# Kernel tuning notes

Hardware: AMD Instinct MI355X
Metric: run time of the kernel (lower is better)

## Reference

```python
import jax, jax.numpy as jnp
import numpy as np

EMBED_DIM = 1024
NUM_HEADS = 16
HEAD_DIM = EMBED_DIM // NUM_HEADS
MLP_SIZE = 4096
LN_EPS = 1e-5


def setup_inputs() -> dict:
    key = jax.random.key(0)
    ks = jax.random.split(key, 12)
    d, f = EMBED_DIM, MLP_SIZE
    s = lambda fan_in: 1.0 / np.sqrt(fan_in)
    return {
        "x": jax.random.normal(ks[0], (2, 2048, d), dtype=jnp.float32),
        "ln1_g": jnp.ones((d,), jnp.float32),
        "ln1_b": jnp.zeros((d,), jnp.float32),
        "ln2_g": jnp.ones((d,), jnp.float32),
        "ln2_b": jnp.zeros((d,), jnp.float32),
        "w_qkv": jax.random.uniform(ks[1], (d, 3 * d), jnp.float32, -s(d), s(d)),
        "b_qkv": jax.random.uniform(ks[2], (3 * d,), jnp.float32, -s(d), s(d)),
        "w_proj": jax.random.uniform(ks[3], (d, d), jnp.float32, -s(d), s(d)),
        "b_proj": jax.random.uniform(ks[4], (d,), jnp.float32, -s(d), s(d)),
        "w_fc1": jax.random.uniform(ks[5], (d, f), jnp.float32, -s(d), s(d)),
        "b_fc1": jax.random.uniform(ks[6], (f,), jnp.float32, -s(d), s(d)),
        "w_fc2": jax.random.uniform(ks[7], (f, d), jnp.float32, -s(f), s(f)),
        "b_fc2": jax.random.uniform(ks[8], (d,), jnp.float32, -s(f), s(f)),
    }


def _layernorm(x, g, b):
    mu = jnp.mean(x, axis=-1, keepdims=True)
    var = jnp.mean(jnp.square(x - mu), axis=-1, keepdims=True)
    return (x - mu) * jax.lax.rsqrt(var + LN_EPS) * g + b


def reference(x, ln1_g, ln1_b, ln2_g, ln2_b, w_qkv, b_qkv, w_proj, b_proj,
              w_fc1, b_fc1, w_fc2, b_fc2):
    B, N, C = x.shape
    H, D = NUM_HEADS, HEAD_DIM
    scale = D ** -0.5

    # --- attention sub-block (pre-LN) ---
    h = _layernorm(x, ln1_g, ln1_b)
    qkv = h @ w_qkv + b_qkv                      # [B,N,3C]
    qkv = qkv.reshape(B, N, 3, H, D)
    q, k, v = (jnp.moveaxis(qkv, 2, 0)[i].transpose(0, 2, 1, 3) for i in range(3))  # each [B,H,N,D]
    attn = jnp.einsum("bhnd,bhmd->bhnm", q, k) * scale
    attn = jax.nn.softmax(attn, axis=-1)
    o = jnp.einsum("bhnm,bhmd->bhnd", attn, v)   # [B,H,N,D]
    o = o.transpose(0, 2, 1, 3).reshape(B, N, C)
    x = x + (o @ w_proj + b_proj)

    # --- MLP sub-block (pre-LN) ---
    h = _layernorm(x, ln2_g, ln2_b)
    h = jax.nn.gelu(h @ w_fc1 + b_fc1, approximate=False)
    x = x + (h @ w_fc2 + b_fc2)
    return x
```

## Files before the change

kernel.cpp:

```cpp
#include <hip/hip_runtime.h>
#include <hip/hip_bf16.h>

typedef __attribute__((ext_vector_type(8))) __bf16 bf16x8;
typedef __attribute__((ext_vector_type(4))) float f32x4;
typedef unsigned short u16;

__device__ __forceinline__ float bf2f(u16 u) {
    unsigned int i = ((unsigned int)u) << 16;
    return __builtin_bit_cast(float, i);
}
__device__ __forceinline__ u16 f2bf_u16(float f) {
    __hip_bfloat16 h = __float2bfloat16(f);
    return *(u16*)&h;
}
__device__ __forceinline__ float gelu_f(float v) {
    return 0.5f * v * (1.0f + erff(v * 0.70710678118654752440f));
}
__device__ __forceinline__ bf16x8 ld_bf8_b64x2(const u16* p) {
    uint2 lo = *(const uint2*)p;
    uint2 hi = *(const uint2*)(p + 4);
    uint4 v = make_uint4(lo.x, lo.y, hi.x, hi.y);
    return __builtin_bit_cast(bf16x8, v);
}
__device__ __forceinline__ void async16(const void* g, void* l) {
    __builtin_amdgcn_global_load_lds(
        (const __attribute__((address_space(1))) void*)g,
        (__attribute__((address_space(3))) void*)l, 16, 0, 0);
}

__global__ void detect_dtype(const void* __restrict__ g1, int* __restrict__ flag) {
    unsigned v = *(const unsigned*)g1;
    *flag = (v == 0x3F800000u) ? 1 : 0;
}

__device__ __forceinline__ void conv8(const void* src, u16* dst, long off, bool f32in) {
    if (f32in) {
        const float* s = (const float*)src + off;
        float4 a = *(const float4*)s, b = *(const float4*)(s + 4);
        u16 o[8] = {f2bf_u16(a.x), f2bf_u16(a.y), f2bf_u16(a.z), f2bf_u16(a.w),
                    f2bf_u16(b.x), f2bf_u16(b.y), f2bf_u16(b.z), f2bf_u16(b.w)};
        *(uint4*)(dst + off) = *(const uint4*)o;
    } else {
        *(uint4*)(dst + off) = *(const uint4*)((const u16*)src + off);
    }
}

__global__ __launch_bounds__(256) void conv_bias(
        const void* __restrict__ bq, const void* __restrict__ bp,
        const void* __restrict__ b1, const void* __restrict__ b2,
        u16* dbq, u16* dbp, u16* db1, u16* db2,
        const int* __restrict__ flag) {
    long e = ((long)blockIdx.x * 256 + threadIdx.x) * 8;
    if (e >= 9216L) return;
    bool f = (*flag != 0);
    if      (e < 3072L) conv8(bq, dbq, e, f);
    else if (e < 4096L) conv8(bp, dbp, e - 3072L, f);
    else if (e < 8192L) conv8(b1, db1, e - 4096L, f);
    else                conv8(b2, db2, e - 8192L, f);
}

__global__ __launch_bounds__(256) void conv_t(const void* __restrict__ src,
                                              u16* __restrict__ dst,
                                              int K, int N,
                                              const int* __restrict__ flag) {
    const bool f32in = (*flag != 0);
    __shared__ u16 T[64 * 68];
    int k0 = blockIdx.y * 64, n0 = blockIdx.x * 64;
    int t = threadIdx.x;
    int kr = t >> 2, nc = (t & 3) * 16;

    u16 tmp[16];
    if (f32in) {
        const float* s = (const float*)src + (size_t)(k0 + kr) * N + n0 + nc;
        float4 a = *(const float4*)s;
        float4 b = *(const float4*)(s + 4);
        float4 c = *(const float4*)(s + 8);
        float4 d = *(const float4*)(s + 12);
        tmp[0]=f2bf_u16(a.x);  tmp[1]=f2bf_u16(a.y);  tmp[2]=f2bf_u16(a.z);  tmp[3]=f2bf_u16(a.w);
        tmp[4]=f2bf_u16(b.x);  tmp[5]=f2bf_u16(b.y);  tmp[6]=f2bf_u16(b.z);  tmp[7]=f2bf_u16(b.w);
        tmp[8]=f2bf_u16(c.x);  tmp[9]=f2bf_u16(c.y);  tmp[10]=f2bf_u16(c.z); tmp[11]=f2bf_u16(c.w);
        tmp[12]=f2bf_u16(d.x); tmp[13]=f2bf_u16(d.y); tmp[14]=f2bf_u16(d.z); tmp[15]=f2bf_u16(d.w);
    } else {
        const u16* s = (const u16*)src + (size_t)(k0 + kr) * N + n0 + nc;
        *(uint4*)&tmp[0] = *(const uint4*)s;
        *(uint4*)&tmp[8] = *(const uint4*)(s + 8);
    }
    u16* dl = &T[kr * 68 + nc];
    #pragma unroll
    for (int j = 0; j < 4; ++j)
        *(uint2*)(dl + 4 * j) = *(const uint2*)&tmp[4 * j];
    __syncthreads();

    int nr = t >> 2, kc = (t & 3) * 16;
    u16 o[16];
    #pragma unroll
    for (int i = 0; i < 16; ++i) o[i] = T[(kc + i) * 68 + nr];
    u16* dp = dst + (size_t)(n0 + nr) * K + k0 + kc;
    *(uint4*)dp       = *(const uint4*)&o[0];
    *(uint4*)(dp + 8) = *(const uint4*)&o[8];
}

__global__ __launch_bounds__(256) void ln_first(const void* __restrict__ xin,
                                                const void* __restrict__ g,
                                                const void* __restrict__ b,
                                                __hip_bfloat16* __restrict__ out,
                                                const int* __restrict__ flag) {
    const bool f32in = (*flag != 0);
    int row = blockIdx.x, t = threadIdx.x;
    size_t base = (size_t)row * 1024 + 4 * t;
    float v[4];
    if (f32in) {
        float4 f = *(const float4*)((const float*)xin + base);
        v[0] = f.x; v[1] = f.y; v[2] = f.z; v[3] = f.w;
    } else {
        ushort4 u = *(const ushort4*)((const __hip_bfloat16*)xin + base);
        v[0] = bf2f(u.x); v[1] = bf2f(u.y); v[2] = bf2f(u.z); v[3] = bf2f(u.w);
    }
    float s = v[0] + v[1] + v[2] + v[3];
    float s2 = v[0]*v[0] + v[1]*v[1] + v[2]*v[2] + v[3]*v[3];
    #pragma unroll
    for (int off = 32; off > 0; off >>= 1) {
        s  += __shfl_down(s, off);
        s2 += __shfl_down(s2, off);
    }
    __shared__ float red[8];
    int wave = t >> 6, lane = t & 63;
    if (lane == 0) { red[wave] = s; red[4 + wave] = s2; }
    __syncthreads();
    float S  = red[0] + red[1] + red[2] + red[3];
    float S2 = red[4] + red[5] + red[6] + red[7];
    float mean = S * (1.0f / 1024.0f);
    float var  = S2 * (1.0f / 1024.0f) - mean * mean;
    float rstd = rsqrtf(var + 1e-5f);
    float gg[4], bb[4];
    if (f32in) {
        float4 fg = *(const float4*)((const float*)g + 4 * t);
        float4 fb = *(const float4*)((const float*)b + 4 * t);
        gg[0]=fg.x; gg[1]=fg.y; gg[2]=fg.z; gg[3]=fg.w;
        bb[0]=fb.x; bb[1]=fb.y; bb[2]=fb.z; bb[3]=fb.w;
    } else {
        ushort4 ug = *(const ushort4*)((const __hip_bfloat16*)g + 4 * t);
        ushort4 ub = *(const ushort4*)((const __hip_bfloat16*)b + 4 * t);
        gg[0]=bf2f(ug.x); gg[1]=bf2f(ug.y); gg[2]=bf2f(ug.z); gg[3]=bf2f(ug.w);
        bb[0]=bf2f(ub.x); bb[1]=bf2f(ub.y); bb[2]=bf2f(ub.z); bb[3]=bf2f(ub.w);
    }
    #pragma unroll
    for (int i = 0; i < 4; ++i)
        out[base + i] = __float2bfloat16((v[i] - mean) * rstd * gg[i] + bb[i]);
}

__global__ __launch_bounds__(256) void ln_mid(const float* __restrict__ x,
                                              const void* __restrict__ g,
                                              const void* __restrict__ b,
                                              __hip_bfloat16* __restrict__ out,
                                              const int* __restrict__ flag) {
    const bool f32in = (*flag != 0);
    int row = blockIdx.x, t = threadIdx.x;
    size_t base = (size_t)row * 1024 + 4 * t;
    float4 f = *(const float4*)(x + base);
    float v[4] = {f.x, f.y, f.z, f.w};
    float s = v[0] + v[1] + v[2] + v[3];
    float s2 = v[0]*v[0] + v[1]*v[1] + v[2]*v[2] + v[3]*v[3];
    #pragma unroll
    for (int off = 32; off > 0; off >>= 1) {
        s  += __shfl_down(s, off);
        s2 += __shfl_down(s2, off);
    }
    __shared__ float red[8];
    int wave = t >> 6, lane = t & 63;
    if (lane == 0) { red[wave] = s; red[4 + wave] = s2; }
    __syncthreads();
    float S  = red[0] + red[1] + red[2] + red[3];
    float S2 = red[4] + red[5] + red[6] + red[7];
    float mean = S * (1.0f / 1024.0f);
    float var  = S2 * (1.0f / 1024.0f) - mean * mean;
    float rstd = rsqrtf(var + 1e-5f);
    float gg[4], bb[4];
    if (f32in) {
        float4 fg = *(const float4*)((const float*)g + 4 * t);
        float4 fb = *(const float4*)((const float*)b + 4 * t);
        gg[0]=fg.x; gg[1]=fg.y; gg[2]=fg.z; gg[3]=fg.w;
        bb[0]=fb.x; bb[1]=fb.y; bb[2]=fb.z; bb[3]=fb.w;
    } else {
        ushort4 ug = *(const ushort4*)((const __hip_bfloat16*)g + 4 * t);
        ushort4 ub = *(const ushort4*)((const __hip_bfloat16*)b + 4 * t);
        gg[0]=bf2f(ug.x); gg[1]=bf2f(ug.y); gg[2]=bf2f(ug.z); gg[3]=bf2f(ug.w);
        bb[0]=bf2f(ub.x); bb[1]=bf2f(ub.y); bb[2]=bf2f(ub.z); bb[3]=bf2f(ub.w);
    }
    #pragma unroll
    for (int i = 0; i < 4; ++i)
        out[base + i] = __float2bfloat16((v[i] - mean) * rstd * gg[i] + bb[i]);
}

template<int EPI, int BN>
__global__ __launch_bounds__(256, 2)
void gemm_bf16(const u16* __restrict__ A,
               const u16* __restrict__ BT,
               const u16* __restrict__ bias,
               const void* __restrict__ res,
               void* __restrict__ outp,
               int M, int N, int K,
               const int* __restrict__ flag) {
    constexpr int NJ = BN / 32;
    constexpr int ASZ = 128 * 32;
    constexpr int BSZ = BN * 32;
    const bool f32in = (*flag != 0);
    __shared__ __align__(16) u16 As[2 * ASZ];
    __shared__ __align__(16) u16 Bs[2 * BSZ];
    (void)M;

    int t = threadIdx.x;
    int w = t >> 6, lane = t & 63;
    int quad = lane >> 4, lq = lane & 15;
    int bm = blockIdx.y * 128, bn = blockIdx.x * BN;
    int wm = (w & 1) * 64, wn = (w >> 1) * (16 * NJ);

    int sr = lane >> 2, sc = (lane & 3) * 8;
    u16* aldst = &As[w * 1024 + lane * 8];
    const u16* ag = A + (size_t)(bm + w * 32 + sr) * K + sc;
    u16* bldst;
    const u16* bg;
    if constexpr (BN == 128) {
        bldst = &Bs[w * 1024 + lane * 8];
        bg = BT + (size_t)(bn + w * 32 + sr) * K + sc;
    } else {
        bldst = &Bs[w * 512 + lane * 8];
        bg = BT + (size_t)(bn + w * 16 + sr) * K + sc;
    }

    f32x4 acc[4][NJ];
    #pragma unroll
    for (int i = 0; i < 4; ++i)
        #pragma unroll
        for (int j = 0; j < NJ; ++j)
            #pragma unroll
            for (int r = 0; r < 4; ++r) acc[i][j][r] = 0.0f;

    async16(ag, aldst);
    async16(ag + (size_t)16 * K, aldst + 512);
    if constexpr (BN == 128) {
        async16(bg, bldst);
        async16(bg + (size_t)16 * K, bldst + 512);
    } else {
        async16(bg, bldst);
    }

    const int nIter = K >> 5;
    for (int k = 0; k < nIter; ++k) {
        __syncthreads();
        int cur = k & 1;
        if (k + 1 < nIter) {
            int nxt = cur ^ 1;
            const u16* agn = ag + (size_t)(k + 1) * 32;
            async16(agn, aldst + nxt * ASZ);
            async16(agn + (size_t)16 * K, aldst + nxt * ASZ + 512);
            if constexpr (BN == 128) {
                const u16* bgn = bg + (size_t)(k + 1) * 32;
                async16(bgn, bldst + nxt * BSZ);
                async16(bgn + (size_t)16 * K, bldst + nxt * BSZ + 512);
            } else {
                async16(bg + (size_t)(k + 1) * 32, bldst + nxt * BSZ);
            }
        }

        const u16* Ac = &As[cur * ASZ];
        const u16* Bc = &Bs[cur * BSZ];
        bf16x8 af[4], bfr[NJ];
        #pragma unroll
        for (int i = 0; i < 4; ++i)
            af[i] = *(const bf16x8*)&Ac[(wm + 16 * i + lq) * 32 + quad * 8];
        #pragma unroll
        for (int j = 0; j < NJ; ++j)
            bfr[j] = *(const bf16x8*)&Bc[(wn + 16 * j + lq) * 32 + quad * 8];
        #pragma unroll
        for (int i = 0; i < 4; ++i)
            #pragma unroll
            for (int j = 0; j < NJ; ++j)
                acc[i][j] = __builtin_amdgcn_mfma_f32_16x16x32_bf16(af[i], bfr[j], acc[i][j], 0, 0, 0);
    }

    #pragma unroll
    for (int i = 0; i < 4; ++i) {
        #pragma unroll
        for (int j = 0; j < NJ; ++j) {
            #pragma unroll
            for (int r = 0; r < 4; ++r) {
                int row = bm + wm + 16 * i + quad * 4 + r;
                int col = bn + wn + 16 * j + lq;
                size_t idx = (size_t)row * N + col;
                float v = acc[i][j][r] + bf2f(bias[col]);
                if constexpr (EPI == 0) {
                    ((__hip_bfloat16*)outp)[idx] = __float2bfloat16(v);
                } else if constexpr (EPI == 1) {
                    v += f32in ? ((const float*)res)[idx]
                               : bf2f(((const u16*)res)[idx]);
                    ((float*)outp)[idx] = v;
                } else if constexpr (EPI == 2) {
                    ((__hip_bfloat16*)outp)[idx] = __float2bfloat16(gelu_f(v));
                } else {
                    v += ((const float*)res)[idx];
                    if (f32in) ((float*)outp)[idx] = v;
                    else       ((__hip_bfloat16*)outp)[idx] = __float2bfloat16(v);
                }
            }
        }
    }
}

__global__ __launch_bounds__(256, 4)
void attn_mfma(const __hip_bfloat16* __restrict__ qkv,
               __hip_bfloat16* __restrict__ o_out) {
    __shared__ __align__(16) u16 Ks[64 * 72];
    __shared__ __align__(16) unsigned int Vt[64 * 36];
    __shared__ __align__(16) u16 Ps[64 * 68];

    int t = threadIdx.x;
    int lane = t & 63, w = t >> 6;
    int quad = lane >> 4, lq = lane & 15;
    int bx = blockIdx.x;
    int b  = bx >> 9, h = (bx >> 5) & 15, qt = bx & 31;
    size_t tok0 = (size_t)b * 2048;

    {
        int key = t >> 2, ld = (t & 3) * 16;
        size_t qb = (tok0 + (size_t)qt * 64 + key) * 3072 + h * 64 + ld;
        uint4 a0 = *(const uint4*)(qkv + qb);
        uint4 a1 = *(const uint4*)(qkv + qb + 8);
        const u16* s0 = (const u16*)&a0;
        const u16* s1 = (const u16*)&a1;
        u16 q16[16];
        #pragma unroll
        for (int j = 0; j < 8; ++j) {
            q16[j]     = f2bf_u16(bf2f(s0[j]) * 0.125f);
            q16[8 + j] = f2bf_u16(bf2f(s1[j]) * 0.125f);
        }
        u16* dst = &Ps[key * 68 + ld];
        #pragma unroll
        for (int j4 = 0; j4 < 4; ++j4)
            *(uint2*)(dst + 4 * j4) = *(const uint2*)&q16[4 * j4];
    }
    __syncthreads();
    bf16x8 qf0 = ld_bf8_b64x2(&Ps[(w * 16 + lq) * 68 + quad * 8]);
    bf16x8 qf1 = ld_bf8_b64x2(&Ps[(w * 16 + lq) * 68 + quad * 8 + 32]);

    f32x4 oacc[4];
    #pragma unroll
    for (int dt = 0; dt < 4; ++dt)
        #pragma unroll
        for (int r = 0; r < 4; ++r) oacc[dt][r] = 0.0f;
    float m_run = -1e30f, l_run = 0.0f;

    int skey = t >> 2, sld = (t & 3) * 16;
    int va = t & 31, vdc = t >> 5;

    for (int kt = 0; kt < 32; ++kt) {
        __syncthreads();
        {
            size_t kb = (tok0 + (size_t)kt * 64 + skey) * 3072 + 1024 + h * 64 + sld;
            uint4 k0 = *(const uint4*)(qkv + kb);
            uint4 k1 = *(const uint4*)(qkv + kb + 8);
            *(uint4*)&Ks[skey * 72 + sld]     = k0;
            *(uint4*)&Ks[skey * 72 + sld + 8] = k1;
        }
        {
            size_t vb = (tok0 + (size_t)kt * 64 + 2 * va) * 3072 + 2048 + h * 64 + vdc * 8;
            uint4 v0 = *(const uint4*)(qkv + vb);
            uint4 v1 = *(const uint4*)(qkv + vb + 3072);
            const u16* p0 = (const u16*)&v0;
            const u16* p1 = (const u16*)&v1;
            #pragma unroll
            for (int j = 0; j < 8; ++j)
                Vt[(vdc * 8 + j) * 36 + va] =
                    (unsigned int)p0[j] | ((unsigned int)p1[j] << 16);
        }
        __syncthreads();

        f32x4 sacc[4];
        #pragma unroll
        for (int j = 0; j < 4; ++j)
            #pragma unroll
            for (int r = 0; r < 4; ++r) sacc[j][r] = 0.0f;
        #pragma unroll
        for (int j = 0; j < 4; ++j) {
            const u16* kr = &Ks[(j * 16 + lq) * 72 + quad * 8];
            bf16x8 kf0 = *(const bf16x8*)kr;
            bf16x8 kf1 = *(const bf16x8*)(kr + 32);
            sacc[j] = __builtin_amdgcn_mfma_f32_16x16x32_bf16(kf0, qf0, sacc[j], 0, 0, 0);
            sacc[j] = __builtin_amdgcn_mfma_f32_16x16x32_bf16(kf1, qf1, sacc[j], 0, 0, 0);
        }

        float mx = sacc[0][0];
        #pragma unroll
        for (int j = 0; j < 4; ++j)
            #pragma unroll
            for (int r = 0; r < 4; ++r) mx = fmaxf(mx, sacc[j][r]);
        mx = fmaxf(mx, __shfl_xor(mx, 16));
        mx = fmaxf(mx, __shfl_xor(mx, 32));
        float mnew = fmaxf(m_run, mx);
        float alpha = __expf(m_run - mnew);

        float ls = 0.0f;
        int prow = (w * 16 + lq) * 68;
        #pragma unroll
        for (int j = 0; j < 4; ++j) {
            float p0 = __expf(sacc[j][0] - mnew);
            float p1 = __expf(sacc[j][1] - mnew);
            float p2 = __expf(sacc[j][2] - mnew);
            float p3 = __expf(sacc[j][3] - mnew);
            ls += (p0 + p1) + (p2 + p3);
            u16 pk[4] = {f2bf_u16(p0), f2bf_u16(p1), f2bf_u16(p2), f2bf_u16(p3)};
            *(uint2*)&Ps[prow + quad * 4 + 16 * j] = *(const uint2*)pk;
        }
        ls += __shfl_xor(ls, 16);
        ls += __shfl_xor(ls, 32);
        l_run = l_run * alpha + ls;
        m_run = mnew;
        #pragma unroll
        for (int dt = 0; dt < 4; ++dt)
            #pragma unroll
            for (int r = 0; r < 4; ++r) oacc[dt][r] *= alpha;

        bf16x8 pf0 = ld_bf8_b64x2(&Ps[prow + quad * 8]);
        bf16x8 pf1 = ld_bf8_b64x2(&Ps[prow + quad * 8 + 32]);
        #pragma unroll
        for (int dt = 0; dt < 4; ++dt) {
            const unsigned int* vr = &Vt[(dt * 16 + lq) * 36 + quad * 4];
            bf16x8 vf0 = __builtin_bit_cast(bf16x8, *(const uint4*)vr);
            bf16x8 vf1 = __builtin_bit_cast(bf16x8, *(const uint4*)(vr + 16));
            oacc[dt] = __builtin_amdgcn_mfma_f32_16x16x32_bf16(vf0, pf0, oacc[dt], 0, 0, 0);
            oacc[dt] = __builtin_amdgcn_mfma_f32_16x16x32_bf16(vf1, pf1, oacc[dt], 0, 0, 0);
        }
    }

    __syncthreads();
    u16* T = Ks;
    float inv = 1.0f / l_run;
    int trow = (w * 16 + lq) * 68;
    #pragma unroll
    for (int dt = 0; dt < 4; ++dt) {
        u16 pk[4] = {f2bf_u16(oacc[dt][0] * inv), f2bf_u16(oacc[dt][1] * inv),
                     f2bf_u16(oacc[dt][2] * inv), f2bf_u16(oacc[dt][3] * inv)};
        *(uint2*)&T[trow + quad * 4 + 16 * dt] = *(const uint2*)pk;
    }
    __syncthreads();
    {
        int q = t >> 2, dc = (t & 3) * 16;
        const u16* src = &T[q * 68 + dc];
        uint2 a0 = *(const uint2*)src;
        uint2 a1 = *(const uint2*)(src + 4);
        uint2 a2 = *(const uint2*)(src + 8);
        uint2 a3 = *(const uint2*)(src + 12);
        u16* op = (u16*)o_out + (tok0 + (size_t)qt * 64 + q) * 1024 + h * 64 + dc;
        *(uint4*)op       = make_uint4(a0.x, a0.y, a1.x, a1.y);
        *(uint4*)(op + 8) = make_uint4(a2.x, a2.y, a3.x, a3.y);
    }
}

extern "C" void kernel_launch(void* const* d_in, const int* in_sizes, int n_in,
                              void* d_out, int out_size, void* d_ws, size_t ws_size,
                              hipStream_t stream) {
    (void)in_sizes; (void)n_in; (void)out_size; (void)ws_size;
    const void* x      = d_in[0];
    const void* ln1_g  = d_in[1];
    const void* ln1_b  = d_in[2];
    const void* ln2_g  = d_in[3];
    const void* ln2_b  = d_in[4];
    const void* w_qkv  = d_in[5];
    const void* b_qkv  = d_in[6];
    const void* w_proj = d_in[7];
    const void* b_proj = d_in[8];
    const void* w_fc1  = d_in[9];
    const void* b_fc1  = d_in[10];
    const void* w_fc2  = d_in[11];
    const void* b_fc2  = d_in[12];

    constexpr int Mtok = 4096;
    char* ws = (char*)d_ws;
    __hip_bfloat16* bufA = (__hip_bfloat16*)ws;
    __hip_bfloat16* qkvb = (__hip_bfloat16*)(ws + ((size_t)8 << 20));
    float*          x1   = (float*)(ws + ((size_t)8 << 20));
    u16*            w1T  = (u16*)(ws + ((size_t)24 << 20));
    u16*            wqT  = (u16*)(ws + ((size_t)32 << 20));
    u16*            wpT  = (u16*)(ws + ((size_t)38 << 20));
    __hip_bfloat16* g1   = (__hip_bfloat16*)(ws + ((size_t)32 << 20));
    u16*            w2T  = (u16*)ws;
    char* BZ = ws + ((size_t)64 << 20);
    u16* bqb = (u16*)BZ;
    u16* bpb = (u16*)(BZ + 8192);
    u16* b1b = (u16*)(BZ + 16384);
    u16* b2b = (u16*)(BZ + 24576);
    int* flag = (int*)(BZ + 32768);

    detect_dtype<<<1, 1, 0, stream>>>(ln1_g, flag);
    conv_bias<<<5, 256, 0, stream>>>(b_qkv, b_proj, b_fc1, b_fc2,
                                     bqb, bpb, b1b, b2b, flag);
    conv_t<<<dim3(3072 / 64, 1024 / 64), 256, 0, stream>>>(w_qkv, wqT, 1024, 3072, flag);
    conv_t<<<dim3(1024 / 64, 1024 / 64), 256, 0, stream>>>(w_proj, wpT, 1024, 1024, flag);
    ln_first<<<Mtok, 256, 0, stream>>>(x, ln1_g, ln1_b, bufA, flag);
    gemm_bf16<0, 128><<<dim3(3072 / 128, Mtok / 128), 256, 0, stream>>>(
        (const u16*)bufA, wqT, bqb, nullptr, qkvb, Mtok, 3072, 1024, flag);
    attn_mfma<<<1024, 256, 0, stream>>>(qkvb, bufA);
    conv_t<<<dim3(4096 / 64, 1024 / 64), 256, 0, stream>>>(w_fc1, w1T, 1024, 4096, flag);
    gemm_bf16<1, 64><<<dim3(1024 / 64, Mtok / 128), 256, 0, stream>>>(
        (const u16*)bufA, wpT, bpb, x, x1, Mtok, 1024, 1024, flag);
    ln_mid<<<Mtok, 256, 0, stream>>>(x1, ln2_g, ln2_b, bufA, flag);
    gemm_bf16<2, 128><<<dim3(4096 / 128, Mtok / 128), 256, 0, stream>>>(
        (const u16*)bufA, w1T, b1b, nullptr, g1, Mtok, 4096, 1024, flag);
    conv_t<<<dim3(1024 / 64, 4096 / 64), 256, 0, stream>>>(w_fc2, w2T, 4096, 1024, flag);
    gemm_bf16<3, 64><<<dim3(1024 / 64, Mtok / 128), 256, 0, stream>>>(
        (const u16*)g1, w2T, b2b, x1, d_out, Mtok, 1024, 4096, flag);
}
```

Baseline: 409.8 us.

## Precompute V transpose, skip softmax rescale, BM=64 tiles for narrow GEMMs

```diff
diff --git a/kernel.cpp b/kernel.cpp
--- a/kernel.cpp
+++ b/kernel.cpp
@@ -16,6 +16,7 @@
 __device__ __forceinline__ float gelu_f(float v) {
     return 0.5f * v * (1.0f + erff(v * 0.70710678118654752440f));
 }
+__device__ __forceinline__ bool is_f32(const unsigned* p) { return *p == 0x3F800000u; }
 __device__ __forceinline__ bf16x8 ld_bf8_b64x2(const u16* p) {
     uint2 lo = *(const uint2*)p;
     uint2 hi = *(const uint2*)(p + 4);
@@ -26,11 +27,6 @@
     __builtin_amdgcn_global_load_lds(
         (const __attribute__((address_space(1))) void*)g,
         (__attribute__((address_space(3))) void*)l, 16, 0, 0);
-}
-
-__global__ void detect_dtype(const void* __restrict__ g1, int* __restrict__ flag) {
-    unsigned v = *(const unsigned*)g1;
-    *flag = (v == 0x3F800000u) ? 1 : 0;
 }
 
 __device__ __forceinline__ void conv8(const void* src, u16* dst, long off, bool f32in) {
@@ -49,10 +45,10 @@
         const void* __restrict__ bq, const void* __restrict__ bp,
         const void* __restrict__ b1, const void* __restrict__ b2,
         u16* dbq, u16* dbp, u16* db1, u16* db2,
-        const int* __restrict__ flag) {
+        const unsigned* __restrict__ dtp) {
     long e = ((long)blockIdx.x * 256 + threadIdx.x) * 8;
     if (e >= 9216L) return;
-    bool f = (*flag != 0);
+    bool f = is_f32(dtp);
     if      (e < 3072L) conv8(bq, dbq, e, f);
     else if (e < 4096L) conv8(bp, dbp, e - 3072L, f);
     else if (e < 8192L) conv8(b1, db1, e - 4096L, f);
@@ -62,8 +58,8 @@
 __global__ __launch_bounds__(256) void conv_t(const void* __restrict__ src,
                                               u16* __restrict__ dst,
                                               int K, int N,
-                                              const int* __restrict__ flag) {
-    const bool f32in = (*flag != 0);
+                                              const unsigned* __restrict__ dtp) {
+    const bool f32in = is_f32(dtp);
     __shared__ u16 T[64 * 68];
     int k0 = blockIdx.y * 64, n0 = blockIdx.x * 64;
     int t = threadIdx.x;
@@ -100,12 +96,33 @@
     *(uint4*)(dp + 8) = *(const uint4*)&o[8];
 }
 
+__global__ __launch_bounds__(256) void vt_prep(const u16* __restrict__ qkv,
+                                               unsigned* __restrict__ vtg) {
+    __shared__ unsigned Vt[64 * 32];
+    int bx = blockIdx.x;
+    int b = bx >> 9, h = (bx >> 5) & 15, kt = bx & 31;
+    int t = threadIdx.x;
+    int va = t & 31, vdc = t >> 5;
+    size_t vb = ((size_t)(b * 2048 + kt * 64 + 2 * va)) * 3072 + 2048 + h * 64 + vdc * 8;
+    uint4 v0 = *(const uint4*)(qkv + vb);
+    uint4 v1 = *(const uint4*)(qkv + vb + 3072);
+    const u16* p0 = (const u16*)&v0;
+    const u16* p1 = (const u16*)&v1;
+    #pragma unroll
+    for (int j = 0; j < 8; ++j)
+        Vt[(vdc * 8 + j) * 32 + va] = (unsigned)p0[j] | ((unsigned)p1[j] << 16);
+    __syncthreads();
+    unsigned* dst = vtg + (size_t)bx * 2048 + t * 8;
+    *(uint4*)dst       = *(const uint4*)&Vt[t * 8];
+    *(uint4*)(dst + 4) = *(const uint4*)&Vt[t * 8 + 4];
+}
+
 __global__ __launch_bounds__(256) void ln_first(const void* __restrict__ xin,
                                                 const void* __restrict__ g,
                                                 const void* __restrict__ b,
                                                 __hip_bfloat16* __restrict__ out,
-                                                const int* __restrict__ flag) {
-    const bool f32in = (*flag != 0);
+                                                const unsigned* __restrict__ dtp) {
+    const bool f32in = is_f32(dtp);
     int row = blockIdx.x, t = threadIdx.x;
     size_t base = (size_t)row * 1024 + 4 * t;
     float v[4];
@@ -153,8 +170,8 @@
                                               const void* __restrict__ g,
                                               const void* __restrict__ b,
                                               __hip_bfloat16* __restrict__ out,
-                                              const int* __restrict__ flag) {
-    const bool f32in = (*flag != 0);
+                                              const unsigned* __restrict__ dtp) {
+    const bool f32in = is_f32(dtp);
     int row = blockIdx.x, t = threadIdx.x;
     size_t base = (size_t)row * 1024 + 4 * t;
     float4 f = *(const float4*)(x + base);
@@ -192,7 +209,7 @@
         out[base + i] = __float2bfloat16((v[i] - mean) * rstd * gg[i] + bb[i]);
 }
 
-template<int EPI, int BN>
+template<int EPI, int BM, int BN>
 __global__ __launch_bounds__(256, 2)
 void gemm_bf16(const u16* __restrict__ A,
                const u16* __restrict__ BT,
@@ -200,11 +217,10 @@
                const void* __restrict__ res,
                void* __restrict__ outp,
                int M, int N, int K,
-               const int* __restrict__ flag) {
-    constexpr int NJ = BN / 32;
-    constexpr int ASZ = 128 * 32;
-    constexpr int BSZ = BN * 32;
-    const bool f32in = (*flag != 0);
+               const unsigned* __restrict__ dtp) {
+    constexpr int NI = BM / 32, NJ = BN / 32;
+    constexpr int ASZ = BM * 32, BSZ = BN * 32;
+    const bool f32in = is_f32(dtp);
     __shared__ __align__(16) u16 As[2 * ASZ];
     __shared__ __align__(16) u16 Bs[2 * BSZ];
     (void)M;
@@ -212,38 +228,27 @@
     int t = threadIdx.x;
     int w = t >> 6, lane = t & 63;
     int quad = lane >> 4, lq = lane & 15;
-    int bm = blockIdx.y * 128, bn = blockIdx.x * BN;
-    int wm = (w & 1) * 64, wn = (w >> 1) * (16 * NJ);
+    int bm = blockIdx.y * BM, bn = blockIdx.x * BN;
+    int wm = (w & 1) * (16 * NI), wn = (w >> 1) * (16 * NJ);
 
     int sr = lane >> 2, sc = (lane & 3) * 8;
-    u16* aldst = &As[w * 1024 + lane * 8];
-    const u16* ag = A + (size_t)(bm + w * 32 + sr) * K + sc;
-    u16* bldst;
-    const u16* bg;
-    if constexpr (BN == 128) {
-        bldst = &Bs[w * 1024 + lane * 8];
-        bg = BT + (size_t)(bn + w * 32 + sr) * K + sc;
-    } else {
-        bldst = &Bs[w * 512 + lane * 8];
-        bg = BT + (size_t)(bn + w * 16 + sr) * K + sc;
-    }
-
-    f32x4 acc[4][NJ];
-    #pragma unroll
-    for (int i = 0; i < 4; ++i)
+    u16* aldst = &As[w * (BM * 8) + lane * 8];
+    const u16* ag = A + (size_t)(bm + w * (BM / 4) + sr) * K + sc;
+    u16* bldst = &Bs[w * (BN * 8) + lane * 8];
+    const u16* bg = BT + (size_t)(bn + w * (BN / 4) + sr) * K + sc;
+
+    f32x4 acc[NI][NJ];
+    #pragma unroll
+    for (int i = 0; i < NI; ++i)
         #pragma unroll
         for (int j = 0; j < NJ; ++j)
             #pragma unroll
             for (int r = 0; r < 4; ++r) acc[i][j][r] = 0.0f;
 
     async16(ag, aldst);
-    async16(ag + (size_t)16 * K, aldst + 512);
-    if constexpr (BN == 128) {
-        async16(bg, bldst);
-        async16(bg + (size_t)16 * K, bldst + 512);
-    } else {
-        async16(bg, bldst);
-    }
+    if constexpr (BM == 128) async16(ag + (size_t)16 * K, aldst + 512);
+    async16(bg, bldst);
+    if constexpr (BN == 128) async16(bg + (size_t)16 * K, bldst + 512);
 
     const int nIter = K >> 5;
     for (int k = 0; k < nIter; ++k) {
@@ -253,34 +258,30 @@
             int nxt = cur ^ 1;
             const u16* agn = ag + (size_t)(k + 1) * 32;
             async16(agn, aldst + nxt * ASZ);
-            async16(agn + (size_t)16 * K, aldst + nxt * ASZ + 512);
-            if constexpr (BN == 128) {
-                const u16* bgn = bg + (size_t)(k + 1) * 32;
-                async16(bgn, bldst + nxt * BSZ);
-                async16(bgn + (size_t)16 * K, bldst + nxt * BSZ + 512);
-            } else {
-                async16(bg + (size_t)(k + 1) * 32, bldst + nxt * BSZ);
-            }
+            if constexpr (BM == 128) async16(agn + (size_t)16 * K, aldst + nxt * ASZ + 512);
+            const u16* bgn = bg + (size_t)(k + 1) * 32;
+            async16(bgn, bldst + nxt * BSZ);
+            if constexpr (BN == 128) async16(bgn + (size_t)16 * K, bldst + nxt * BSZ + 512);
         }
 
         const u16* Ac = &As[cur * ASZ];
         const u16* Bc = &Bs[cur * BSZ];
-        bf16x8 af[4], bfr[NJ];
-        #pragma unroll
-        for (int i = 0; i < 4; ++i)
+        bf16x8 af[NI], bfr[NJ];
+        #pragma unroll
+        for (int i = 0; i < NI; ++i)
             af[i] = *(const bf16x8*)&Ac[(wm + 16 * i + lq) * 32 + quad * 8];
         #pragma unroll
         for (int j = 0; j < NJ; ++j)
             bfr[j] = *(const bf16x8*)&Bc[(wn + 16 * j + lq) * 32 + quad * 8];
         #pragma unroll
-        for (int i = 0; i < 4; ++i)
+        for (int i = 0; i < NI; ++i)
             #pragma unroll
             for (int j = 0; j < NJ; ++j)
                 acc[i][j] = __builtin_amdgcn_mfma_f32_16x16x32_bf16(af[i], bfr[j], acc[i][j], 0, 0, 0);
     }
 
     #pragma unroll
-    for (int i = 0; i < 4; ++i) {
+    for (int i = 0; i < NI; ++i) {
         #pragma unroll
         for (int j = 0; j < NJ; ++j) {
             #pragma unroll
@@ -309,9 +310,10 @@
 
 __global__ __launch_bounds__(256, 4)
 void attn_mfma(const __hip_bfloat16* __restrict__ qkv,
+               const unsigned* __restrict__ vtg,
                __hip_bfloat16* __restrict__ o_out) {
     __shared__ __align__(16) u16 Ks[64 * 72];
-    __shared__ __align__(16) unsigned int Vt[64 * 36];
+    __shared__ __align__(16) unsigned Vt[64 * 36];
     __shared__ __align__(16) u16 Ps[64 * 68];
 
     int t = threadIdx.x;
@@ -351,7 +353,7 @@
     float m_run = -1e30f, l_run = 0.0f;
 
     int skey = t >> 2, sld = (t & 3) * 16;
-    int va = t & 31, vdc = t >> 5;
+    int vrow = t >> 2, vcol = (t & 3) * 8;
 
     for (int kt = 0; kt < 32; ++kt) {
         __syncthreads();
@@ -363,15 +365,12 @@
             *(uint4*)&Ks[skey * 72 + sld + 8] = k1;
         }
         {
-            size_t vb = (tok0 + (size_t)kt * 64 + 2 * va) * 3072 + 2048 + h * 64 + vdc * 8;
-            uint4 v0 = *(const uint4*)(qkv + vb);
-            uint4 v1 = *(const uint4*)(qkv + vb + 3072);
-            const u16* p0 = (const u16*)&v0;
-            const u16* p1 = (const u16*)&v1;
-            #pragma unroll
-            for (int j = 0; j < 8; ++j)
-                Vt[(vdc * 8 + j) * 36 + va] =
-                    (unsigned int)p0[j] | ((unsigned int)p1[j] << 16);
+            const unsigned* vg = vtg + ((size_t)(b * 512 + h * 32 + kt)) * 2048 + t * 8;
+            uint4 w0 = *(const uint4*)vg;
+            uint4 w1 = *(const uint4*)(vg + 4);
+            unsigned* vdst = &Vt[vrow * 36 + vcol];
+            *(uint4*)vdst       = w0;
+            *(uint4*)(vdst + 4) = w1;
         }
         __syncthreads();
 
@@ -397,7 +396,15 @@
         mx = fmaxf(mx, __shfl_xor(mx, 16));
         mx = fmaxf(mx, __shfl_xor(mx, 32));
         float mnew = fmaxf(m_run, mx);
-        float alpha = __expf(m_run - mnew);
+        if (__any(mnew > m_run)) {
+            float alpha = __expf(m_run - mnew);
+            l_run *= alpha;
+            #pragma unroll
+            for (int dt = 0; dt < 4; ++dt)
+                #pragma unroll
+                for (int r = 0; r < 4; ++r) oacc[dt][r] *= alpha;
+        }
+        m_run = mnew;
 
         float ls = 0.0f;
         int prow = (w * 16 + lq) * 68;
@@ -413,18 +420,13 @@
         }
         ls += __shfl_xor(ls, 16);
         ls += __shfl_xor(ls, 32);
-        l_run = l_run * alpha + ls;
-        m_run = mnew;
-        #pragma unroll
-        for (int dt = 0; dt < 4; ++dt)
-            #pragma unroll
-            for (int r = 0; r < 4; ++r) oacc[dt][r] *= alpha;
+        l_run += ls;
 
         bf16x8 pf0 = ld_bf8_b64x2(&Ps[prow + quad * 8]);
         bf16x8 pf1 = ld_bf8_b64x2(&Ps[prow + quad * 8 + 32]);
         #pragma unroll
         for (int dt = 0; dt < 4; ++dt) {
-            const unsigned int* vr = &Vt[(dt * 16 + lq) * 36 + quad * 4];
+            const unsigned* vr = &Vt[(dt * 16 + lq) * 36 + quad * 4];
             bf16x8 vf0 = __builtin_bit_cast(bf16x8, *(const uint4*)vr);
             bf16x8 vf1 = __builtin_bit_cast(bf16x8, *(const uint4*)(vr + 16));
             oacc[dt] = __builtin_amdgcn_mfma_f32_16x16x32_bf16(vf0, pf0, oacc[dt], 0, 0, 0);
@@ -473,6 +475,7 @@
     const void* b_fc1  = d_in[10];
     const void* w_fc2  = d_in[11];
     const void* b_fc2  = d_in[12];
+    const unsigned* probe = (const unsigned*)ln1_g;
 
     constexpr int Mtok = 4096;
     char* ws = (char*)d_ws;
@@ -482,6 +485,7 @@
     u16*            w1T  = (u16*)(ws + ((size_t)24 << 20));
     u16*            wqT  = (u16*)(ws + ((size_t)32 << 20));
     u16*            wpT  = (u16*)(ws + ((size_t)38 << 20));
+    unsigned*       vtg  = (unsigned*)(ws + ((size_t)40 << 20));
     __hip_bfloat16* g1   = (__hip_bfloat16*)(ws + ((size_t)32 << 20));
     u16*            w2T  = (u16*)ws;
     char* BZ = ws + ((size_t)64 << 20);
@@ -489,24 +493,23 @@
     u16* bpb = (u16*)(BZ + 8192);
     u16* b1b = (u16*)(BZ + 16384);
     u16* b2b = (u16*)(BZ + 24576);
-    int* flag = (int*)(BZ + 32768);
-
-    detect_dtype<<<1, 1, 0, stream>>>(ln1_g, flag);
+
     conv_bias<<<5, 256, 0, stream>>>(b_qkv, b_proj, b_fc1, b_fc2,
-                                     bqb, bpb, b1b, b2b, flag);
-    conv_t<<<dim3(3072 / 64, 1024 / 64), 256, 0, stream>>>(w_qkv, wqT, 1024, 3072, flag);
-    conv_t<<<dim3(1024 / 64, 1024 / 64), 256, 0, stream>>>(w_proj, wpT, 1024, 1024, flag);
-    ln_first<<<Mtok, 256, 0, stream>>>(x, ln1_g, ln1_b, bufA, flag);
-    gemm_bf16<0, 128><<<dim3(3072 / 128, Mtok / 128), 256, 0, stream>>>(
-        (const u16*)bufA, wqT, bqb, nullptr, qkvb, Mtok, 3072, 1024, flag);
-    attn_mfma<<<1024, 256, 0, stream>>>(qkvb, bufA);
-    conv_t<<<dim3(4096 / 64, 1024 / 64), 256, 0, stream>>>(w_fc1, w1T, 1024, 4096, flag);
-    gemm_bf16<1, 64><<<dim3(1024 / 64, Mtok / 128), 256, 0, stream>>>(
-        (const u16*)bufA, wpT, bpb, x, x1, Mtok, 1024, 1024, flag);
-    ln_mid<<<Mtok, 256, 0, stream>>>(x1, ln2_g, ln2_b, bufA, flag);
-    gemm_bf16<2, 128><<<dim3(4096 / 128, Mtok / 128), 256, 0, stream>>>(
-        (const u16*)bufA, w1T, b1b, nullptr, g1, Mtok, 4096, 1024, flag);
-    conv_t<<<dim3(1024 / 64, 4096 / 64), 256, 0, stream>>>(w_fc2, w2T, 4096, 1024, flag);
-    gemm_bf16<3, 64><<<dim3(1024 / 64, Mtok / 128), 256, 0, stream>>>(
-        (const u16*)g1, w2T, b2b, x1, d_out, Mtok, 1024, 4096, flag);
-}
+                                     bqb, bpb, b1b, b2b, probe);
+    conv_t<<<dim3(3072 / 64, 1024 / 64), 256, 0, stream>>>(w_qkv, wqT, 1024, 3072, probe);
+    conv_t<<<dim3(1024 / 64, 1024 / 64), 256, 0, stream>>>(w_proj, wpT, 1024, 1024, probe);
+    ln_first<<<Mtok, 256, 0, stream>>>(x, ln1_g, ln1_b, bufA, probe);
+    gemm_bf16<0, 128, 128><<<dim3(3072 / 128, Mtok / 128), 256, 0, stream>>>(
+        (const u16*)bufA, wqT, bqb, nullptr, qkvb, Mtok, 3072, 1024, probe);
+    vt_prep<<<1024, 256, 0, stream>>>((const u16*)qkvb, vtg);
+    attn_mfma<<<1024, 256, 0, stream>>>(qkvb, vtg, bufA);
+    conv_t<<<dim3(4096 / 64, 1024 / 64), 256, 0, stream>>>(w_fc1, w1T, 1024, 4096, probe);
+    gemm_bf16<1, 64, 64><<<dim3(1024 / 64, Mtok / 64), 256, 0, stream>>>(
+        (const u16*)bufA, wpT, bpb, x, x1, Mtok, 1024, 1024, probe);
+    ln_mid<<<Mtok, 256, 0, stream>>>(x1, ln2_g, ln2_b, bufA, probe);
+    gemm_bf16<2, 128, 128><<<dim3(4096 / 128, Mtok / 128), 256, 0, stream>>>(
+        (const u16*)bufA, w1T, b1b, nullptr, g1, Mtok, 4096, 1024, probe);
+    conv_t<<<dim3(1024 / 64, 4096 / 64), 256, 0, stream>>>(w_fc2, w2T, 4096, 1024, probe);
+    gemm_bf16<3, 64, 64><<<dim3(1024 / 64, Mtok / 64), 256, 0, stream>>>(
+        (const u16*)g1, w2T, b2b, x1, d_out, Mtok, 1024, 4096, probe);
+}
```

Result: faster. 395.0 us (-3.6%).
